# Performance work log

Measured on AMD Instinct MI355X. Metric: run time of the kernel, lower is better.

The kernel has to match this reference:

```python
import jax, jax.numpy as jnp
import numpy as np

B, NQ, NK, QS, KS, H, VD = 16, 64, 512, 256, 256, 256, 256


def setup_inputs() -> dict:
    key = jax.random.key(0)
    k1, k2, k3, k4, k5, k6, k7 = jax.random.split(key, 7)
    return {
        "queries": jax.random.normal(k1, (B, NQ, QS), dtype=jnp.float32),
        "keys": jax.random.normal(k2, (B, NK, KS), dtype=jnp.float32),
        "values": jax.random.normal(k3, (B, NK, VD), dtype=jnp.float32),
        "valid_lens": jax.random.randint(k4, (B,), 1, NK + 1, dtype=jnp.int32),
        # learned params (nn.Linear with bias=False): W_q [QS,H], W_k [KS,H], w_v [H]
        "W_q": jax.random.normal(k5, (QS, H), dtype=jnp.float32) / np.sqrt(QS),
        "W_k": jax.random.normal(k6, (KS, H), dtype=jnp.float32) / np.sqrt(KS),
        "w_v": jax.random.normal(k7, (H,), dtype=jnp.float32) / np.sqrt(H),
    }


def reference(queries, keys, values, valid_lens, W_q, W_k, w_v):
    # project: q [B,nq,H], k [B,nk,H]
    q = jnp.einsum("bqd,dh->bqh", queries, W_q)
    k = jnp.einsum("bkd,dh->bkh", keys, W_k)
    # broadcast-add -> tanh -> score reduction via w_v: [B,nq,nk]
    features = jnp.tanh(q[:, :, None, :] + k[:, None, :, :])  # [B,nq,nk,H]
    scores = jnp.einsum("bqkh,h->bqk", features, w_v)
    # masked softmax over keys (positions >= valid_len masked out)
    mask = jnp.arange(scores.shape[-1])[None, None, :] < valid_lens[:, None, None]
    scores = jnp.where(mask, scores, -1e6)
    attn = jax.nn.softmax(scores, axis=-1)
    # weighted sum of values (dropout p=0 / eval mode => identity)
    return jnp.einsum("bqk,bkv->bqv", attn, values)
```

## Files before the change

### kernel.cpp

```cpp
#include <hip/hip_runtime.h>
#include <hip/hip_bf16.h>

#define BB 16
#define NQ 64
#define NK 512
#define HD 256

typedef __attribute__((ext_vector_type(8))) short short8;
typedef __attribute__((ext_vector_type(4))) float f32x4;

__device__ __forceinline__ ushort bf16_rne(float v) {
    unsigned u = __float_as_uint(v);
    return (ushort)((u + 0x7FFFu + ((u >> 16) & 1u)) >> 16);
}
__device__ __forceinline__ float bf16_to_f(ushort h) {
    return __uint_as_float(((unsigned)h) << 16);
}

__global__ __launch_bounds__(256) void wconv(
    const float* __restrict__ wq, const float* __restrict__ wk,
    ushort* __restrict__ wqh, ushort* __restrict__ wql,
    ushort* __restrict__ wkh, ushort* __restrict__ wkl)
{
    int widx = blockIdx.x * 256 + threadIdx.x;
    const float* W; ushort *wh, *wl;
    if (widx < 16384) { W = wq; wh = wqh; wl = wql; }
    else { W = wk; wh = wkh; wl = wkl; widx -= 16384; }
    int n  = widx >> 6;
    int k4 = (widx & 63) * 4;
    ushort hh[4], ll[4];
    #pragma unroll
    for (int c = 0; c < 4; ++c) {
        float v = W[(k4 + c) * 256 + n];
        hh[c] = bf16_rne(v);
        ll[c] = bf16_rne(v - bf16_to_f(hh[c]));
    }
    *(ushort4*)&wh[n * 256 + k4] = make_ushort4(hh[0], hh[1], hh[2], hh[3]);
    *(ushort4*)&wl[n * 256 + k4] = make_ushort4(ll[0], ll[1], ll[2], ll[3]);
}

__global__ __launch_bounds__(256, 2) void proj_fused(
    const float* __restrict__ queries, const float* __restrict__ keys,
    const ushort* __restrict__ wqh, const ushort* __restrict__ wql,
    const ushort* __restrict__ wkh, const ushort* __restrict__ wkl,
    float* __restrict__ qp, float* __restrict__ kp, float scale)
{
    __shared__ ushort AsH[64 * 64], AsL[64 * 64];
    __shared__ ushort BsH[64 * 64], BsL[64 * 64];

    const float* A; const ushort *Bh, *Bl; float* C; int rows0;
    const int bx = blockIdx.x;
    if (bx < 16) { A = queries; Bh = wqh; Bl = wql; C = qp; rows0 = bx * 64; }
    else         { A = keys;    Bh = wkh; Bl = wkl; C = kp; rows0 = (bx - 16) * 64; }
    const int cols0 = blockIdx.y * 64;

    const int t = threadIdx.x, lane = t & 63, wave = t >> 6;
    const int quad = lane >> 4, l15 = lane & 15;
    const int sr  = t >> 2;
    const int sc2 = (t & 3) * 2;

    f32x4 acc[4];
    #pragma unroll
    for (int j = 0; j < 4; ++j) acc[j] = (f32x4){0.f, 0.f, 0.f, 0.f};

    for (int k0 = 0; k0 < 256; k0 += 64) {
        const float* arow = &A[(size_t)(rows0 + sr) * 256 + k0 + sc2 * 8];
        float4 a0 = *(const float4*)&arow[0];
        float4 a1 = *(const float4*)&arow[4];
        float4 a2 = *(const float4*)&arow[8];
        float4 a3 = *(const float4*)&arow[12];
        const ushort* bhp = &Bh[(size_t)(cols0 + sr) * 256 + k0 + sc2 * 8];
        const ushort* blp = &Bl[(size_t)(cols0 + sr) * 256 + k0 + sc2 * 8];
        short8 b0h = *(const short8*)&bhp[0];
        short8 b1h = *(const short8*)&bhp[8];
        short8 b0l = *(const short8*)&blp[0];
        short8 b1l = *(const short8*)&blp[8];

        __syncthreads();

        float av[16] = {a0.x, a0.y, a0.z, a0.w, a1.x, a1.y, a1.z, a1.w,
                        a2.x, a2.y, a2.z, a2.w, a3.x, a3.y, a3.z, a3.w};
        short8 ah0, ah1, al0, al1;
        #pragma unroll
        for (int e = 0; e < 8; ++e) {
            ushort h0 = bf16_rne(av[e]);
            ushort h1 = bf16_rne(av[8 + e]);
            ah0[e] = (short)h0;
            ah1[e] = (short)h1;
            al0[e] = (short)bf16_rne(av[e] - bf16_to_f(h0));
            al1[e] = (short)bf16_rne(av[8 + e] - bf16_to_f(h1));
        }
        {
            int s0 = sr * 8 + ((sc2 + 0) ^ (sr & 7));
            int s1 = sr * 8 + ((sc2 + 1) ^ (sr & 7));
            *(short8*)&AsH[s0 * 8] = ah0;
            *(short8*)&AsH[s1 * 8] = ah1;
            *(short8*)&AsL[s0 * 8] = al0;
            *(short8*)&AsL[s1 * 8] = al1;
            *(short8*)&BsH[s0 * 8] = b0h;
            *(short8*)&BsH[s1 * 8] = b1h;
            *(short8*)&BsL[s0 * 8] = b0l;
            *(short8*)&BsL[s1 * 8] = b1l;
        }
        __syncthreads();

        #pragma unroll
        for (int ks = 0; ks < 2; ++ks) {
            const int c = ks * 4 + quad;
            short8 aH, aL, bH[4], bL[4];
            {
                int r = wave * 16 + l15;
                int slot = r * 8 + (c ^ (r & 7));
                aH = *(const short8*)&AsH[slot * 8];
                aL = *(const short8*)&AsL[slot * 8];
            }
            #pragma unroll
            for (int ns = 0; ns < 4; ++ns) {
                int n = ns * 16 + l15;
                int slot = n * 8 + (c ^ (n & 7));
                bH[ns] = *(const short8*)&BsH[slot * 8];
                bL[ns] = *(const short8*)&BsL[slot * 8];
            }
            #pragma unroll
            for (int ns = 0; ns < 4; ++ns)
                acc[ns] = __builtin_amdgcn_mfma_f32_16x16x32_bf16(aH, bH[ns], acc[ns], 0, 0, 0);
            #pragma unroll
            for (int ns = 0; ns < 4; ++ns)
                acc[ns] = __builtin_amdgcn_mfma_f32_16x16x32_bf16(aL, bH[ns], acc[ns], 0, 0, 0);
            #pragma unroll
            for (int ns = 0; ns < 4; ++ns)
                acc[ns] = __builtin_amdgcn_mfma_f32_16x16x32_bf16(aH, bL[ns], acc[ns], 0, 0, 0);
        }
    }

    const int rbase = rows0 + wave * 16 + quad * 4;
    #pragma unroll
    for (int ns = 0; ns < 4; ++ns) {
        int col = cols0 + ns * 16 + l15;
        #pragma unroll
        for (int r = 0; r < 4; ++r)
            C[(size_t)(rbase + r) * 256 + col] =
                __builtin_amdgcn_exp2f(acc[ns][r] * scale);
    }
}

__global__ __launch_bounds__(512, 4) void score_pv_seg3(
    const float* __restrict__ qp,
    const float* __restrict__ kp,
    const float* __restrict__ values,
    const int*   __restrict__ vlens,
    const float* __restrict__ w_v,
    float* __restrict__ pO,
    float* __restrict__ pM,
    float* __restrict__ pL)
{
    __shared__ float eq[8][260];
    __shared__ float wv[HD];
    __shared__ float Ps[8][66];
    __shared__ float sP[8][66];
    __shared__ float part[4][8][260];

    const int b   = blockIdx.x & 15;
    const int qt  = blockIdx.x >> 4;
    const int seg = blockIdx.y;
    const int vl  = vlens[b];
    if (seg * 64 >= vl) return;

    const int t = threadIdx.x, lane = t & 63, wave = t >> 6;
    const int kq = wave & 3;
    const int hh = wave >> 2;
    const int key = kq * 16 + (lane >> 2);
    const int ch  = lane & 3;
    const int kg  = seg * 64 + key;

    const float* krow = kp + ((size_t)b * NK + kg) * HD + hh * 128 + ch * 4;
    float4 ek[8];
    #pragma unroll
    for (int j = 0; j < 8; ++j) ek[j] = *(const float4*)&krow[j * 16];

    const float* qsrc = qp + ((size_t)b * NQ + qt * 8) * HD;
    {
        int row = t >> 6, c4 = (t & 63) * 4;
        *(float4*)&eq[row][c4] = *(const float4*)&qsrc[(size_t)row * HD + c4];
    }
    if (t < 64) *(float4*)&wv[t * 4] = *(const float4*)&w_v[t * 4];
    __syncthreads();

    float Wsum;
    {
        float ws = wv[lane] + wv[lane + 64] + wv[lane + 128] + wv[lane + 192];
        #pragma unroll
        for (int off = 32; off; off >>= 1) ws += __shfl_xor(ws, off);
        Wsum = ws;
    }

    float s[8] = {0.f, 0.f, 0.f, 0.f, 0.f, 0.f, 0.f, 0.f};
    #pragma unroll
    for (int j = 0; j < 8; ++j) {
        const int h = hh * 128 + j * 16 + ch * 4;
        float4 e4 = ek[j];
        float4 w4 = *(const float4*)&wv[h];
        #pragma unroll
        for (int qi = 0; qi < 8; ++qi) {
            float4 q4 = *(const float4*)&eq[qi][h];
            float p0 = fmaf(q4.x, e4.x, 1.f);
            float p1 = fmaf(q4.y, e4.y, 1.f);
            float p2 = fmaf(q4.z, e4.z, 1.f);
            float p3 = fmaf(q4.w, e4.w, 1.f);
            float d01 = p0 * p1;
            float d23 = p2 * p3;
            float n01 = fmaf(w4.x, p1, w4.y * p0);
            float n23 = fmaf(w4.z, p3, w4.w * p2);
            float num = fmaf(d01, n23, d23 * n01);
            float r   = __builtin_amdgcn_rcpf(d01 * d23);
            s[qi] = fmaf(num, r, s[qi]);
        }
    }
    #pragma unroll
    for (int qi = 0; qi < 8; ++qi) {
        s[qi] += __shfl_xor(s[qi], 1);
        s[qi] += __shfl_xor(s[qi], 2);
    }
    if (hh == 1 && ch == 0) {
        #pragma unroll
        for (int qi = 0; qi < 8; ++qi) sP[qi][key] = s[qi];
    }
    __syncthreads();
    if (hh == 0 && ch == 0) {
        const bool masked = (kg >= vl);
        #pragma unroll
        for (int qi = 0; qi < 8; ++qi)
            Ps[qi][key] = masked ? -1e6f
                                 : fmaf(-2.f, s[qi] + sP[qi][key], Wsum);
    }
    __syncthreads();

    const float L2E = 1.4426950408889634f;
    {
        const int row = wave;
        float sv = Ps[row][lane];
        float m = sv;
        #pragma unroll
        for (int off = 32; off; off >>= 1) m = fmaxf(m, __shfl_xor(m, off));
        float e = __builtin_amdgcn_exp2f((sv - m) * L2E);
        float l = e;
        #pragma unroll
        for (int off = 32; off; off >>= 1) l += __shfl_xor(l, off);
        Ps[row][lane] = e;
        if (lane == 0) {
            size_t mi = (((size_t)(b * 8 + qt) * 8 + seg)) * 8 + row;
            pM[mi] = m;
            pL[mi] = l;
        }
    }
    __syncthreads();

    f32x4 acc[4];
    #pragma unroll
    for (int r = 0; r < 4; ++r) acc[r] = (f32x4){0.f, 0.f, 0.f, 0.f};
    const float* vbase = values + ((size_t)b * NK + seg * 64 + kq * 16) * HD;
    #pragma unroll
    for (int i = 0; i < 16; ++i) {
        float4 v = *(const float4*)&vbase[(size_t)i * HD + lane * 4];
        #pragma unroll
        for (int r = 0; r < 4; ++r) {
            float p = Ps[hh * 4 + r][kq * 16 + i];
            acc[r][0] = fmaf(p, v.x, acc[r][0]);
            acc[r][1] = fmaf(p, v.y, acc[r][1]);
            acc[r][2] = fmaf(p, v.z, acc[r][2]);
            acc[r][3] = fmaf(p, v.w, acc[r][3]);
        }
    }
    #pragma unroll
    for (int r = 0; r < 4; ++r)
        *(f32x4*)&part[kq][hh * 4 + r][lane * 4] = acc[r];
    __syncthreads();

    const size_t ob = (((size_t)(b * 8 + qt) * 8 + seg)) * 8 * 256;
    {
        int qi = t >> 6, c4 = (t & 63) * 4;
        float4 p0 = *(const float4*)&part[0][qi][c4];
        float4 p1 = *(const float4*)&part[1][qi][c4];
        float4 p2 = *(const float4*)&part[2][qi][c4];
        float4 p3 = *(const float4*)&part[3][qi][c4];
        float4 o;
        o.x = (p0.x + p1.x) + (p2.x + p3.x);
        o.y = (p0.y + p1.y) + (p2.y + p3.y);
        o.z = (p0.z + p1.z) + (p2.z + p3.z);
        o.w = (p0.w + p1.w) + (p2.w + p3.w);
        *(float4*)&pO[ob + (size_t)qi * 256 + c4] = o;
    }
}

__global__ __launch_bounds__(256) void combine_seg2(
    const float* __restrict__ pO, const float* __restrict__ pM,
    const float* __restrict__ pL, const int* __restrict__ vlens,
    float* __restrict__ out)
{
    const int b  = blockIdx.x >> 6;
    const int q  = blockIdx.x & 63;
    const int t  = threadIdx.x;
    const int vl = vlens[b];
    const int nc = (vl + 63) >> 6;
    const int qt = q >> 3, qi = q & 7;
    const float L2E = 1.4426950408889634f;

    const size_t base = (size_t)(b * 8 + qt) * 8;

    float mi[8], li[8];
    float m = -3e38f;
    #pragma unroll
    for (int i = 0; i < 8; ++i) {
        if (i < nc) {
            mi[i] = pM[(base + i) * 8 + qi];
            li[i] = pL[(base + i) * 8 + qi];
            m = fmaxf(m, mi[i]);
        }
    }
    float L = 0.f, wi[8];
    #pragma unroll
    for (int i = 0; i < 8; ++i) {
        if (i < nc) {
            wi[i] = __builtin_amdgcn_exp2f((mi[i] - m) * L2E);
            L = fmaf(li[i], wi[i], L);
        }
    }
    float acc = 0.f;
    #pragma unroll
    for (int i = 0; i < 8; ++i) {
        if (i < nc) acc = fmaf(wi[i], pO[((base + i) * 8 + qi) * 256 + t], acc);
    }
    out[((size_t)(b * 64 + q)) * 256 + t] = acc * __builtin_amdgcn_rcpf(L);
}

extern "C" void kernel_launch(void* const* d_in, const int* in_sizes, int n_in,
                              void* d_out, int out_size, void* d_ws, size_t ws_size,
                              hipStream_t stream) {
    const float* queries = (const float*)d_in[0];
    const float* keys    = (const float*)d_in[1];
    const float* values  = (const float*)d_in[2];
    const int*   vlens   = (const int*)d_in[3];
    const float* W_q     = (const float*)d_in[4];
    const float* W_k     = (const float*)d_in[5];
    const float* w_v     = (const float*)d_in[6];
    float* out = (float*)d_out;

    float*  kp  = (float*)d_ws;
    float*  qp  = kp + (size_t)BB * NK * HD;
    float*  pO  = qp + (size_t)BB * NQ * HD;
    float*  pM  = pO + (size_t)BB * 8 * 8 * 8 * 256;
    float*  pL  = pM + (size_t)BB * 8 * 8 * 8;
    ushort* wqh = (ushort*)(pL + (size_t)BB * 8 * 8 * 8);
    ushort* wql = wqh + 65536;
    ushort* wkh = wql + 65536;
    ushort* wkl = wkh + 65536;

    const float SC = 2.885390081777927f;

    wconv<<<dim3(128), 256, 0, stream>>>(W_q, W_k, wqh, wql, wkh, wkl);
    proj_fused<<<dim3(144, 4), 256, 0, stream>>>(queries, keys,
                                                 wqh, wql, wkh, wkl,
                                                 qp, kp, SC);
    score_pv_seg3<<<dim3(128, 8), 512, 0, stream>>>(qp, kp, values, vlens, w_v,
                                                    pO, pM, pL);
    combine_seg2<<<dim3(BB * NQ), 256, 0, stream>>>(pO, pM, pL, vlens, out);
}
```

Measured before the change: 111.5 us.

## Drop softmax max-subtraction using bounded scores; prefetch values; simplify combine

Scores are bounded because they are sums of w_v-weighted tanh terms, so the kernel exponentiates them directly without a per-segment max. This removes the max reduction, one barrier, the pM buffer, and the rescaling in the combine kernel, which now just sums partial outputs and denominators. Value rows are prefetched four iterations ahead into registers, and the launch-bounds occupancy hint is raised from 4 to 6. In exchange it relies on the score magnitude staying small enough that exp cannot overflow, and the extra prefetch registers press against the higher occupancy target.

```diff
diff --git a/kernel.cpp b/kernel.cpp
--- a/kernel.cpp
+++ b/kernel.cpp
@@ -144,14 +144,13 @@
     }
 }
 
-__global__ __launch_bounds__(512, 4) void score_pv_seg3(
+__global__ __launch_bounds__(512, 6) void score_pv_seg5(
     const float* __restrict__ qp,
     const float* __restrict__ kp,
     const float* __restrict__ values,
     const int*   __restrict__ vlens,
     const float* __restrict__ w_v,
     float* __restrict__ pO,
-    float* __restrict__ pM,
     float* __restrict__ pL)
 {
     __shared__ float eq[8][260];
@@ -226,42 +225,39 @@
         for (int qi = 0; qi < 8; ++qi) sP[qi][key] = s[qi];
     }
     __syncthreads();
+    const float L2E = 1.4426950408889634f;
     if (hh == 0 && ch == 0) {
         const bool masked = (kg >= vl);
         #pragma unroll
-        for (int qi = 0; qi < 8; ++qi)
-            Ps[qi][key] = masked ? -1e6f
-                                 : fmaf(-2.f, s[qi] + sP[qi][key], Wsum);
+        for (int qi = 0; qi < 8; ++qi) {
+            float sv = fmaf(-2.f, s[qi] + sP[qi][key], Wsum);
+            Ps[qi][key] = masked ? 0.f : __builtin_amdgcn_exp2f(sv * L2E);
+        }
     }
     __syncthreads();
 
-    const float L2E = 1.4426950408889634f;
+    const float* vbase = values + ((size_t)b * NK + seg * 64 + kq * 16) * HD;
+    float4 vv[4];
+    #pragma unroll
+    for (int i = 0; i < 4; ++i)
+        vv[i] = *(const float4*)&vbase[(size_t)i * HD + lane * 4];
+
     {
-        const int row = wave;
-        float sv = Ps[row][lane];
-        float m = sv;
-        #pragma unroll
-        for (int off = 32; off; off >>= 1) m = fmaxf(m, __shfl_xor(m, off));
-        float e = __builtin_amdgcn_exp2f((sv - m) * L2E);
-        float l = e;
+        float l = Ps[wave][lane];
         #pragma unroll
         for (int off = 32; off; off >>= 1) l += __shfl_xor(l, off);
-        Ps[row][lane] = e;
-        if (lane == 0) {
-            size_t mi = (((size_t)(b * 8 + qt) * 8 + seg)) * 8 + row;
-            pM[mi] = m;
-            pL[mi] = l;
-        }
-    }
-    __syncthreads();
+        if (lane == 0)
+            pL[(((size_t)(b * 8 + qt) * 8 + seg)) * 8 + wave] = l;
+    }
 
     f32x4 acc[4];
     #pragma unroll
     for (int r = 0; r < 4; ++r) acc[r] = (f32x4){0.f, 0.f, 0.f, 0.f};
-    const float* vbase = values + ((size_t)b * NK + seg * 64 + kq * 16) * HD;
     #pragma unroll
     for (int i = 0; i < 16; ++i) {
-        float4 v = *(const float4*)&vbase[(size_t)i * HD + lane * 4];
+        float4 v = vv[i & 3];
+        if (i + 4 < 16)
+            vv[i & 3] = *(const float4*)&vbase[(size_t)(i + 4) * HD + lane * 4];
         #pragma unroll
         for (int r = 0; r < 4; ++r) {
             float p = Ps[hh * 4 + r][kq * 16 + i];
@@ -292,43 +288,25 @@
     }
 }
 
-__global__ __launch_bounds__(256) void combine_seg2(
-    const float* __restrict__ pO, const float* __restrict__ pM,
-    const float* __restrict__ pL, const int* __restrict__ vlens,
-    float* __restrict__ out)
+__global__ __launch_bounds__(256) void combine_seg3(
+    const float* __restrict__ pO, const float* __restrict__ pL,
+    const int* __restrict__ vlens, float* __restrict__ out)
 {
     const int b  = blockIdx.x >> 6;
     const int q  = blockIdx.x & 63;
     const int t  = threadIdx.x;
-    const int vl = vlens[b];
-    const int nc = (vl + 63) >> 6;
+    const int nc = (vlens[b] + 63) >> 6;
     const int qt = q >> 3, qi = q & 7;
-    const float L2E = 1.4426950408889634f;
 
     const size_t base = (size_t)(b * 8 + qt) * 8;
 
-    float mi[8], li[8];
-    float m = -3e38f;
+    float L = 0.f, acc = 0.f;
     #pragma unroll
     for (int i = 0; i < 8; ++i) {
         if (i < nc) {
-            mi[i] = pM[(base + i) * 8 + qi];
-            li[i] = pL[(base + i) * 8 + qi];
-            m = fmaxf(m, mi[i]);
-        }
-    }
-    float L = 0.f, wi[8];
-    #pragma unroll
-    for (int i = 0; i < 8; ++i) {
-        if (i < nc) {
-            wi[i] = __builtin_amdgcn_exp2f((mi[i] - m) * L2E);
-            L = fmaf(li[i], wi[i], L);
-        }
-    }
-    float acc = 0.f;
-    #pragma unroll
-    for (int i = 0; i < 8; ++i) {
-        if (i < nc) acc = fmaf(wi[i], pO[((base + i) * 8 + qi) * 256 + t], acc);
+            L   += pL[(base + i) * 8 + qi];
+            acc += pO[((base + i) * 8 + qi) * 256 + t];
+        }
     }
     out[((size_t)(b * 64 + q)) * 256 + t] = acc * __builtin_amdgcn_rcpf(L);
 }
@@ -348,8 +326,7 @@
     float*  kp  = (float*)d_ws;
     float*  qp  = kp + (size_t)BB * NK * HD;
     float*  pO  = qp + (size_t)BB * NQ * HD;
-    float*  pM  = pO + (size_t)BB * 8 * 8 * 8 * 256;
-    float*  pL  = pM + (size_t)BB * 8 * 8 * 8;
+    float*  pL  = pO + (size_t)BB * 8 * 8 * 8 * 256;
     ushort* wqh = (ushort*)(pL + (size_t)BB * 8 * 8 * 8);
     ushort* wql = wqh + 65536;
     ushort* wkh = wql + 65536;
@@ -361,7 +338,7 @@
     proj_fused<<<dim3(144, 4), 256, 0, stream>>>(queries, keys,
                                                  wqh, wql, wkh, wkl,
                                                  qp, kp, SC);
-    score_pv_seg3<<<dim3(128, 8), 512, 0, stream>>>(qp, kp, values, vlens, w_v,
-                                                    pO, pM, pL);
-    combine_seg2<<<dim3(BB * NQ), 256, 0, stream>>>(pO, pM, pL, vlens, out);
-}
+    score_pv_seg5<<<dim3(128, 8), 512, 0, stream>>>(qp, kp, values, vlens, w_v,
+                                                    pO, pL);
+    combine_seg3<<<dim3(BB * NQ), 256, 0, stream>>>(pO, pL, vlens, out);
+}
```

Measured after the change: 110.4 us. Within noise of the previous version (-1.0%).
